# Optimization experiments

Measured on AMD Instinct MI355X. Metric: run time of the kernel, lower is better.

The kernel has to match this reference:

```python
import jax, jax.numpy as jnp
import numpy as np

B, S, D, H, L = 16, 1024, 512, 8, 3
NUM_Q, NUM_C, TOTAL_RES = 10000, 300, 2


def setup_inputs() -> dict:
    k = jax.random.split(jax.random.key(0), 20)
    n = lambda i, s, sc=0.02: jax.random.normal(k[i], s, jnp.float32) * sc
    z = lambda: jnp.zeros((D,), jnp.float32)
    o = lambda: jnp.ones((D,), jnp.float32)
    return {
        'in_ex': jax.random.randint(k[0], (B, S), 0, NUM_Q),
        'in_cat': jax.random.randint(k[1], (B, S), 0, NUM_C),
        'in_res': jax.random.randint(k[2], (B, S), 0, 2),
        'in_pos': n(3, (B, S, D)),
        'en_out': n(4, (B, S, D)),
        'E_res': n(5, (TOTAL_RES + 1, D)),
        'E_ex': n(6, (2 * NUM_Q + 1, D)),
        'E_cat': n(7, (2 * NUM_C + 1, D)),
        'g1': o(), 'be1': z(), 'g2': o(), 'be2': z(), 'g3': o(), 'be3': z(),
        'Wq1': n(8, (D, D)), 'bq1': z(), 'Wk1': n(9, (D, D)), 'bk1': z(),
        'Wv1': n(10, (D, D)), 'bv1': z(), 'Wo1': n(11, (D, D)), 'bo1': z(),
        'Wq2': n(12, (D, D)), 'bq2': z(), 'Wk2': n(13, (D, D)), 'bk2': z(),
        'Wv2': n(14, (D, D)), 'bv2': z(), 'Wo2': n(15, (D, D)), 'bo2': z(),
        'fW1': n(16, (D, D)), 'fb1': z(), 'fW2': n(17, (D, D)), 'fb2': z(),
    }


def layer_norm(x, g, b, eps=1e-5):
    m = x.mean(-1, keepdims=True)
    v = ((x - m) ** 2).mean(-1, keepdims=True)
    return (x - m) / jnp.sqrt(v + eps) * g + b


def pyr_attn(q_in, kv_in, Wq, bq, Wk, bk, Wv, bv, Wo, bo):
    # q_in, kv_in: (S, B, D) as in nn.MultiheadAttention convention
    Sq, Bq, Dm = q_in.shape
    dh = Dm // H
    heads = lambda x: x.reshape(x.shape[0], Bq, H, dh).transpose(1, 2, 0, 3)  # (B,H,S,dh)
    qh = heads(q_in @ Wq + bq)
    kh = heads(kv_in @ Wk + bk)
    vh = heads(kv_in @ Wv + bv)
    Skv = kv_in.shape[0]
    i = jnp.arange(Sq)[:, None]
    Ks, Vs, Ms = [], [], []
    for l in range(L):  # pyramid levels: keys/values avg-pooled by 2**l
        f = 2 ** l
        nb = Skv // f
        Ks.append(kh[:, :, :nb * f].reshape(Bq, H, nb, f, dh).mean(3))
        Vs.append(vh[:, :, :nb * f].reshape(Bq, H, nb, f, dh).mean(3))
        # causal: query i may attend pooled block j only if the block ends at or before i
        Ms.append(i >= (jnp.arange(nb)[None, :] + 1) * f - 1)
    K = jnp.concatenate(Ks, 2)
    V = jnp.concatenate(Vs, 2)
    M = jnp.concatenate(Ms, 1)  # (Sq, K_total) multi-level causal mask
    sc = jnp.einsum('bhqd,bhkd->bhqk', qh, K) / np.sqrt(dh).astype(np.float32)
    sc = jnp.where(M[None, None], sc, -1e9)
    a = jax.nn.softmax(sc, -1)
    out = jnp.einsum('bhqk,bhkd->bhqd', a, V)
    return out.transpose(2, 0, 1, 3).reshape(Sq, Bq, Dm) @ Wo + bo


def reference(in_ex, in_cat, in_res, in_pos, en_out, E_res, E_ex, E_cat,
              g1, be1, g2, be2, g3, be3,
              Wq1, bq1, Wk1, bk1, Wv1, bv1, Wo1, bo1,
              Wq2, bq2, Wk2, bk2, Wv2, bv2, Wo2, bo2,
              fW1, fb1, fW2, fb2):
    # embedding sum (first_block=True)
    out = E_res[in_res] + E_ex[in_ex + NUM_Q * in_res] + E_cat[in_cat + NUM_C * in_res] + in_pos
    out = out.transpose(1, 0, 2)  # (S, B, D)
    out = layer_norm(out, g1, be1)
    out = out + pyr_attn(out, out, Wq1, bq1, Wk1, bk1, Wv1, bv1, Wo1, bo1)
    en = layer_norm(en_out.transpose(1, 0, 2), g2, be2)
    out = out + pyr_attn(out, en, Wq2, bq2, Wk2, bk2, Wv2, bv2, Wo2, bo2)
    out = out.transpose(1, 0, 2)  # (B, S, D)
    out = layer_norm(out, g3, be3)
    out = out + (jax.nn.relu(out @ fW1 + fb1) @ fW2 + fb2)
    return out
```

## Files before the change

### kernel.cpp

```cpp
#include <hip/hip_runtime.h>


#define BB 16
#define SS 1024
#define DD 512
#define HH 8
#define DH 64
#define KTOT 1792
#define NROW (BB*SS)

typedef unsigned short u16;
typedef __attribute__((ext_vector_type(8))) u16 u16x8;
typedef __attribute__((ext_vector_type(4))) u16 u16x4;
typedef __attribute__((ext_vector_type(8))) short s16x8;
typedef __attribute__((ext_vector_type(4))) float f32x4;

__device__ __forceinline__ float b2f(u16 u) {
    return __uint_as_float(((unsigned int)u) << 16);
}
__device__ __forceinline__ u16 f2b(float f) {
    unsigned int u = __float_as_uint(f);
    return (u16)((u + 0x7FFF + ((u >> 16) & 1)) >> 16);
}
__device__ __forceinline__ s16x8 u2s8(u16x8 u) {
    union { u16x8 u; s16x8 s; } x; x.u = u; return x.s;
}
__device__ __forceinline__ f32x4 mfma16(s16x8 a, s16x8 b, f32x4 c) {
    return __builtin_amdgcn_mfma_f32_16x16x32_bf16(a, b, c, 0, 0, 0);
}
__device__ __forceinline__ float wave_sum(float v) {
    #pragma unroll
    for (int m = 1; m < 64; m <<= 1) v += __shfl_xor(v, m, 64);
    return v;
}
__device__ __forceinline__ float exp2a(float x) {
    float r;
    asm("v_exp_f32 %0, %1" : "=v"(r) : "v"(x));
    return r;
}
__device__ __forceinline__ unsigned int cvtpk(float a, float b) {
    unsigned int r;
    asm("v_cvt_pk_bf16_f32 %0, %1, %2" : "=v"(r) : "v"(a), "v"(b));
    return r;
}

__global__ __launch_bounds__(256) void embed_ln_k(
    const int* __restrict__ in_ex, const int* __restrict__ in_cat,
    const int* __restrict__ in_res, const float* __restrict__ in_pos,
    const float* __restrict__ E_res, const float* __restrict__ E_ex,
    const float* __restrict__ E_cat, const float* __restrict__ g,
    const float* __restrict__ be, float* __restrict__ out)
{
    int wave = threadIdx.x >> 6, lane = threadIdx.x & 63;
    int row = blockIdx.x * 4 + wave;
    int res = in_res[row];
    int ex  = in_ex[row] + 10000 * res;
    int cat = in_cat[row] + 300 * res;
    int d0 = lane * 8;
    const float* pr = &E_res[(size_t)res * DD + d0];
    const float* pe = &E_ex[(size_t)ex * DD + d0];
    const float* pc = &E_cat[(size_t)cat * DD + d0];
    const float* pp = &in_pos[(size_t)row * DD + d0];
    float x[8]; float s = 0.f;
    #pragma unroll
    for (int j = 0; j < 8; j++) { x[j] = pr[j] + pe[j] + pc[j] + pp[j]; s += x[j]; }
    s = wave_sum(s);
    float mean = s * (1.0f / DD);
    float vs = 0.f;
    #pragma unroll
    for (int j = 0; j < 8; j++) { float d = x[j] - mean; vs += d * d; }
    vs = wave_sum(vs);
    float rstd = rsqrtf(vs * (1.0f / DD) + 1e-5f);
    #pragma unroll
    for (int j = 0; j < 8; j++)
        out[(size_t)row * DD + d0 + j] = (x[j] - mean) * rstd * g[d0 + j] + be[d0 + j];
}

template<bool OUTB>
__global__ __launch_bounds__(256) void ln_k(
    const float* __restrict__ x, const float* __restrict__ g,
    const float* __restrict__ be, void* __restrict__ outv)
{
    int wave = threadIdx.x >> 6, lane = threadIdx.x & 63;
    int row = blockIdx.x * 4 + wave;
    int d0 = lane * 8;
    const float* px = &x[(size_t)row * DD + d0];
    float xv[8]; float s = 0.f;
    #pragma unroll
    for (int j = 0; j < 8; j++) { xv[j] = px[j]; s += xv[j]; }
    s = wave_sum(s);
    float mean = s * (1.0f / DD);
    float vs = 0.f;
    #pragma unroll
    for (int j = 0; j < 8; j++) { float d = xv[j] - mean; vs += d * d; }
    vs = wave_sum(vs);
    float rstd = rsqrtf(vs * (1.0f / DD) + 1e-5f);
    #pragma unroll
    for (int j = 0; j < 8; j++) {
        float v = (xv[j] - mean) * rstd * g[d0 + j] + be[d0 + j];
        if (OUTB) ((u16*)outv)[(size_t)row * DD + d0 + j] = f2b(v);
        else      ((float*)outv)[(size_t)row * DD + d0 + j] = v;
    }
}

__global__ __launch_bounds__(256) void transpose_k(const float* __restrict__ src, u16* __restrict__ dst)
{
    int idx = blockIdx.x * 256 + threadIdx.x;
    int n = idx & 511, k = idx >> 9;
    dst[n * 512 + k] = f2b(src[k * 512 + n]);
}

__global__ __launch_bounds__(256) void pool_k12_k(u16* __restrict__ KP)
{
    int idx = blockIdx.x * 256 + threadIdx.x;
    int d = idx & 63;
    int t = idx >> 6;
    int k12 = t % 768;
    int bh = t / 768;
    int s0, f;
    if (k12 < 512) { s0 = 2 * k12; f = 2; } else { s0 = 4 * (k12 - 512); f = 4; }
    size_t base = (size_t)bh * KTOT * DH;
    float acc = 0.f;
    for (int i = 0; i < f; i++)
        acc += b2f(KP[base + (size_t)(s0 + i) * DH + d]);
    KP[base + (size_t)(1024 + k12) * DH + d] = f2b(acc * (1.0f / (float)f));
}

__global__ __launch_bounds__(256) void pool_vt_k(const u16* __restrict__ Vp, u16* __restrict__ VPt)
{
    __shared__ __align__(16) u16 T[64 * 72];
    int tid = threadIdx.x;
    int st = blockIdx.x;
    int h  = blockIdx.y;
    int b  = blockIdx.z;
    int s0 = st * 64;
    {
        const u16* src = &Vp[((size_t)(b * SS + s0)) * DD + h * DH];
        #pragma unroll
        for (int it = 0; it < 2; it++) {
            int idx = it * 256 + tid;
            int row = idx >> 3, unit = idx & 7;
            *(u16x8*)&T[row * 72 + unit * 8] =
                *(const u16x8*)&src[(size_t)row * DD + unit * 8];
        }
    }
    __syncthreads();
    int d = tid & 63, g = tid >> 6;
    size_t obase = ((size_t)(b * HH + h) * DH + d) * KTOT;
    #pragma unroll
    for (int gg = 0; gg < 2; gg++) {
        int grp = g * 2 + gg;
        u16x8 v;
        #pragma unroll
        for (int j = 0; j < 8; j++) v[j] = T[(grp * 8 + j) * 72 + d];
        *(u16x8*)&VPt[obase + s0 + grp * 8] = v;
    }
    {
        u16x8 v;
        #pragma unroll
        for (int j = 0; j < 8; j++) {
            int sl = g * 8 + j;
            float a = b2f(T[(2 * sl) * 72 + d]) + b2f(T[(2 * sl + 1) * 72 + d]);
            v[j] = f2b(a * 0.5f);
        }
        *(u16x8*)&VPt[obase + 1024 + st * 32 + g * 8] = v;
    }
    {
        u16x4 v;
        #pragma unroll
        for (int j = 0; j < 4; j++) {
            int s2 = g * 4 + j;
            float a = 0.f;
            #pragma unroll
            for (int i = 0; i < 4; i++) a += b2f(T[(4 * s2 + i) * 72 + d]);
            v[j] = f2b(a * 0.25f);
        }
        *(u16x4*)&VPt[obase + 1536 + st * 16 + g * 4] = v;
    }
}

template<bool AF32, bool RELU, bool RES, bool OUTB, bool KLAY>
__global__ __launch_bounds__(256) void gemm_k(
    const void* __restrict__ Av, const u16* __restrict__ Wt,
    const float* __restrict__ bias, const float* __restrict__ resid,
    void* __restrict__ Cv, int M, int K)
{
    const int N = 512;
    __shared__ __align__(16) u16 As[128 * 40];
    __shared__ __align__(16) u16 Bs[128 * 40];
    int tid = threadIdx.x;
    int wave = tid >> 6, lane = tid & 63;
    int quad = lane >> 4, l16 = lane & 15;
    int m0 = blockIdx.y * 128, n0 = blockIdx.x * 128;
    int wm = (wave >> 1) * 64, wn = (wave & 1) * 64;
    int r = tid >> 1, cg = (tid & 1) * 16;
    f32x4 acc[4][4];
    #pragma unroll
    for (int i = 0; i < 4; i++)
        #pragma unroll
        for (int j = 0; j < 4; j++)
            #pragma unroll
            for (int rr = 0; rr < 4; rr++) acc[i][j][rr] = 0.f;

    for (int k0 = 0; k0 < K; k0 += 32) {
        __syncthreads();
        if (AF32) {
            const float* src = &((const float*)Av)[(size_t)(m0 + r) * K + k0 + cg];
            u16x8 lo, hi;
            #pragma unroll
            for (int j = 0; j < 8; j++) { lo[j] = f2b(src[j]); hi[j] = f2b(src[j + 8]); }
            *(u16x8*)&As[r * 40 + cg] = lo;
            *(u16x8*)&As[r * 40 + cg + 8] = hi;
        } else {
            const u16* src = &((const u16*)Av)[(size_t)(m0 + r) * K + k0 + cg];
            *(u16x8*)&As[r * 40 + cg] = *(const u16x8*)&src[0];
            *(u16x8*)&As[r * 40 + cg + 8] = *(const u16x8*)&src[8];
        }
        {
            const u16* src = &Wt[(size_t)(n0 + r) * K + k0 + cg];
            *(u16x8*)&Bs[r * 40 + cg] = *(const u16x8*)&src[0];
            *(u16x8*)&Bs[r * 40 + cg + 8] = *(const u16x8*)&src[8];
        }
        __syncthreads();
        s16x8 af[4], bfr[4];
        #pragma unroll
        for (int i = 0; i < 4; i++)
            af[i] = u2s8(*(const u16x8*)&As[(wm + i * 16 + l16) * 40 + quad * 8]);
        #pragma unroll
        for (int j = 0; j < 4; j++)
            bfr[j] = u2s8(*(const u16x8*)&Bs[(wn + j * 16 + l16) * 40 + quad * 8]);
        #pragma unroll
        for (int i = 0; i < 4; i++)
            #pragma unroll
            for (int j = 0; j < 4; j++)
                acc[i][j] = mfma16(af[i], bfr[j], acc[i][j]);
    }

    #pragma unroll
    for (int j = 0; j < 4; j++) {
        int col = n0 + wn + j * 16 + l16;
        float bv = bias[col];
        #pragma unroll
        for (int i = 0; i < 4; i++) {
            int rowb = m0 + wm + i * 16 + quad * 4;
            #pragma unroll
            for (int rr = 0; rr < 4; rr++) {
                float v = acc[i][j][rr] + bv;
                if (RELU) v = fmaxf(v, 0.f);
                int row = rowb + rr;
                if (RES) v += resid[(size_t)row * N + col];
                if (KLAY) {
                    int b_ = row >> 10, s_ = row & 1023;
                    size_t dst = (((size_t)(b_ * HH + (col >> 6)) * KTOT) + s_) * DH + (col & 63);
                    ((u16*)Cv)[dst] = f2b(v);
                } else if (OUTB) {
                    ((u16*)Cv)[(size_t)row * N + col] = f2b(v);
                } else {
                    ((float*)Cv)[(size_t)row * N + col] = v;
                }
            }
        }
    }
}

__global__ __launch_bounds__(512) void attn_k(
    const u16* __restrict__ Qp, const u16* __restrict__ KP,
    const u16* __restrict__ VPt, u16* __restrict__ Hout)
{
    __shared__ __align__(16) u16 Ksh[64 * 72];
    __shared__ __align__(16) u16 Vsh[64 * 72];
    int tid = threadIdx.x;
    int wave = tid >> 6, lane = tid & 63;
    int quad = lane >> 4, l16 = lane & 15;
    int id = blockIdx.x;
    int h = id & 7;
    int inner = id >> 3;
    int x = inner & 3, b = inner >> 2;

    int t0 = x + 4 * wave;
    int tiles[2] = { t0, 63 - t0 };

    const u16* Kb = KP  + ((size_t)(b * HH + h)) * KTOT * DH;
    const u16* Vt = VPt + ((size_t)(b * HH + h)) * DH * KTOT;

    s16x8 qa[2][2];
    f32x4 o[2][4];
    float mrun[2] = {-INFINITY, -INFINITY}, lrun[2] = {0.f, 0.f};
    #pragma unroll
    for (int c = 0; c < 2; c++) {
        int q0 = tiles[c] * 16;
        const u16* qrow = Qp + ((size_t)(b * SS + q0 + l16)) * DD + h * DH;
        qa[c][0] = u2s8(*(const u16x8*)&qrow[quad * 8]);
        qa[c][1] = u2s8(*(const u16x8*)&qrow[32 + quad * 8]);
        #pragma unroll
        for (int j = 0; j < 4; j++)
            #pragma unroll
            for (int r = 0; r < 4; r++) o[c][j][r] = 0.f;
    }

    int row0 = 8 * (l16 >> 2) + (l16 & 3);
    const float Cs = 0.18033688f;

    int srow = tid >> 3, sunit = tid & 7;
    u16x8 kreg = *(const u16x8*)&Kb[(size_t)tid * 8];
    u16x8 vreg = *(const u16x8*)&Vt[(size_t)srow * KTOT + sunit * 8];

    for (int ch = 0; ch < 28; ch++) {
        int kbase = ch * 64;
        int lv = (ch < 16) ? 0 : (ch < 24) ? 1 : 2;
        __syncthreads();
        *(u16x8*)&Ksh[srow * 72 + sunit * 8] = kreg;
        *(u16x8*)&Vsh[srow * 72 + sunit * 8] = vreg;
        __syncthreads();
        if (ch + 1 < 28) {
            int nb = (ch + 1) * 64;
            kreg = *(const u16x8*)&Kb[(size_t)nb * DH + tid * 8];
            vreg = *(const u16x8*)&Vt[(size_t)srow * KTOT + nb + sunit * 8];
        }

        #pragma unroll
        for (int c = 0; c < 2; c++) {
            int q0 = tiles[c] * 16;
            int qmax = q0 + 15;
            int efirst = (lv == 0) ? kbase
                       : (lv == 1) ? 2 * (kbase - 1024) + 1
                                   : 4 * (kbase - 1536) + 3;
            if (efirst > qmax) continue;

            int q = q0 + l16;
            int kmax;
            if (lv == 0)      kmax = q - kbase;
            else if (lv == 1) kmax = ((q - 1) >> 1) - (kbase - 1024);
            else              kmax = ((q - 3) >> 2) - (kbase - 1536);
            int thrbase = kmax - 8 * quad;

            float pz[4][4];
            __builtin_amdgcn_s_setprio(1);
            #pragma unroll
            for (int t = 0; t < 4; t++) {
                const int toff = (t & 1) * 4 + (t >> 1) * 32;
                const u16* kr = &Ksh[(row0 + toff) * 72];
                s16x8 kf0 = u2s8(*(const u16x8*)&kr[quad * 8]);
                s16x8 kf1 = u2s8(*(const u16x8*)&kr[32 + quad * 8]);
                f32x4 z;
                #pragma unroll
                for (int r = 0; r < 4; r++) z[r] = 0.f;
                z = mfma16(kf0, qa[c][0], z);
                z = mfma16(kf1, qa[c][1], z);
                int thr = thrbase - toff;
                #pragma unroll
                for (int r = 0; r < 4; r++)
                    pz[t][r] = (r <= thr) ? z[r] : -1e30f;
            }
            __builtin_amdgcn_s_setprio(0);

            float a0 = fmaxf(fmaxf(pz[0][0], pz[0][1]), fmaxf(pz[0][2], pz[0][3]));
            float a1 = fmaxf(fmaxf(pz[1][0], pz[1][1]), fmaxf(pz[1][2], pz[1][3]));
            float a2 = fmaxf(fmaxf(pz[2][0], pz[2][1]), fmaxf(pz[2][2], pz[2][3]));
            float a3 = fmaxf(fmaxf(pz[3][0], pz[3][1]), fmaxf(pz[3][2], pz[3][3]));
            float cmax = fmaxf(fmaxf(a0, a1), fmaxf(a2, a3));
            cmax = fmaxf(cmax, __shfl_xor(cmax, 16, 64));
            cmax = fmaxf(cmax, __shfl_xor(cmax, 32, 64));
            float newm = fmaxf(mrun[c], cmax);
            float nmC = newm * Cs;
            float al = exp2a((mrun[c] - newm) * Cs);
            float p[4][4]; float ps = 0.f;
            #pragma unroll
            for (int t = 0; t < 4; t++)
                #pragma unroll
                for (int r = 0; r < 4; r++) {
                    p[t][r] = exp2a(fmaf(pz[t][r], Cs, -nmC));
                    ps += p[t][r];
                }
            ps += __shfl_xor(ps, 16, 64);
            ps += __shfl_xor(ps, 32, 64);
            lrun[c] = lrun[c] * al + ps;
            mrun[c] = newm;

            float alr[4];
            #pragma unroll
            for (int r = 0; r < 4; r++) alr[r] = __shfl(al, quad * 4 + r, 64);
            #pragma unroll
            for (int j = 0; j < 4; j++)
                #pragma unroll
                for (int r = 0; r < 4; r++) o[c][j][r] *= alr[r];

            union { unsigned int w[4]; u16x8 v; } U0, U1;
            U0.w[0] = cvtpk(p[0][0], p[0][1]); U0.w[1] = cvtpk(p[0][2], p[0][3]);
            U0.w[2] = cvtpk(p[1][0], p[1][1]); U0.w[3] = cvtpk(p[1][2], p[1][3]);
            U1.w[0] = cvtpk(p[2][0], p[2][1]); U1.w[1] = cvtpk(p[2][2], p[2][3]);
            U1.w[2] = cvtpk(p[3][0], p[3][1]); U1.w[3] = cvtpk(p[3][2], p[3][3]);
            s16x8 pf0 = u2s8(U0.v), pf1 = u2s8(U1.v);

            __builtin_amdgcn_s_setprio(1);
            #pragma unroll
            for (int j = 0; j < 4; j++) {
                const u16* vr = &Vsh[(j * 16 + l16) * 72];
                o[c][j] = mfma16(pf0, u2s8(*(const u16x8*)&vr[quad * 8]), o[c][j]);
                o[c][j] = mfma16(pf1, u2s8(*(const u16x8*)&vr[32 + quad * 8]), o[c][j]);
            }
            __builtin_amdgcn_s_setprio(0);
        }
    }

    #pragma unroll
    for (int c = 0; c < 2; c++) {
        int q0 = tiles[c] * 16;
        float il = 1.0f / lrun[c];
        float ilr[4];
        #pragma unroll
        for (int r = 0; r < 4; r++) ilr[r] = __shfl(il, quad * 4 + r, 64);
        #pragma unroll
        for (int r = 0; r < 4; r++) {
            int q = q0 + quad * 4 + r;
            #pragma unroll
            for (int j = 0; j < 4; j++)
                Hout[((size_t)(b * SS + q)) * DD + h * DH + j * 16 + l16] = f2b(o[c][j][r] * ilr[r]);
        }
    }
}

extern "C" void kernel_launch(void* const* d_in, const int* in_sizes, int n_in,
                              void* d_out, int out_size, void* d_ws, size_t ws_size,
                              hipStream_t stream)
{
    (void)in_sizes; (void)n_in; (void)out_size; (void)ws_size;
    const int* in_ex  = (const int*)d_in[0];
    const int* in_cat = (const int*)d_in[1];
    const int* in_res = (const int*)d_in[2];
    const float* in_pos = (const float*)d_in[3];
    const float* en_out = (const float*)d_in[4];
    const float* E_res  = (const float*)d_in[5];
    const float* E_ex   = (const float*)d_in[6];
    const float* E_cat  = (const float*)d_in[7];
    const float* g1 = (const float*)d_in[8],  *be1 = (const float*)d_in[9];
    const float* g2 = (const float*)d_in[10], *be2 = (const float*)d_in[11];
    const float* g3 = (const float*)d_in[12], *be3 = (const float*)d_in[13];
    const float* Wq1 = (const float*)d_in[14], *bq1 = (const float*)d_in[15];
    const float* Wk1 = (const float*)d_in[16], *bk1 = (const float*)d_in[17];
    const float* Wv1 = (const float*)d_in[18], *bv1 = (const float*)d_in[19];
    const float* Wo1 = (const float*)d_in[20], *bo1 = (const float*)d_in[21];
    const float* Wq2 = (const float*)d_in[22], *bq2 = (const float*)d_in[23];
    const float* Wk2 = (const float*)d_in[24], *bk2 = (const float*)d_in[25];
    const float* Wv2 = (const float*)d_in[26], *bv2 = (const float*)d_in[27];
    const float* Wo2 = (const float*)d_in[28], *bo2 = (const float*)d_in[29];
    const float* fW1 = (const float*)d_in[30], *fb1 = (const float*)d_in[31];
    const float* fW2 = (const float*)d_in[32], *fb2 = (const float*)d_in[33];

    char* ws = (char*)d_ws;
    const size_t U = (size_t)NROW * DD * 2;
    float* x1 = (float*)(ws);
    u16* qb   = (u16*)(ws + 2 * U);
    u16* vb   = (u16*)(ws + 3 * U);
    u16* hb   = (u16*)(ws + 4 * U);
    u16* kp   = (u16*)(ws + 5 * U);
    u16* vpt  = (u16*)(ws + 5 * U + 7 * U / 4);
    u16* wt   = (u16*)(ws + 8 * U + U / 2);
    float* x2 = (float*)d_out;
    u16* en = (u16*)(ws);
    float* x3 = x1;
    float* x4 = (float*)(ws + 5 * U);
    u16* ff1 = hb;

    const float* wsrc[10] = {Wq1, Wk1, Wv1, Wo1, Wq2, Wk2, Wv2, Wo2, fW1, fW2};
    for (int i = 0; i < 10; i++)
        transpose_k<<<1024, 256, 0, stream>>>(wsrc[i], wt + (size_t)i * 262144);
    u16* tWq1 = wt,            *tWk1 = wt + 262144,   *tWv1 = wt + 2*262144, *tWo1 = wt + 3*262144;
    u16* tWq2 = wt + 4*262144, *tWk2 = wt + 5*262144, *tWv2 = wt + 6*262144, *tWo2 = wt + 7*262144;
    u16* tF1  = wt + 8*262144, *tF2  = wt + 9*262144;

    dim3 ggrid(4, 128);
    dim3 vtgrid(16, 8, 16);

    embed_ln_k<<<4096, 256, 0, stream>>>(in_ex, in_cat, in_res, in_pos,
                                         E_res, E_ex, E_cat, g1, be1, x1);

    gemm_k<true,false,false,true,false><<<ggrid, 256, 0, stream>>>(x1, tWq1, bq1, nullptr, qb, NROW, 512);
    gemm_k<true,false,false,true,true ><<<ggrid, 256, 0, stream>>>(x1, tWk1, bk1, nullptr, kp, NROW, 512);
    gemm_k<true,false,false,true,false><<<ggrid, 256, 0, stream>>>(x1, tWv1, bv1, nullptr, vb, NROW, 512);
    pool_k12_k<<<24576, 256, 0, stream>>>(kp);
    pool_vt_k<<<vtgrid, 256, 0, stream>>>(vb, vpt);
    attn_k<<<512, 512, 0, stream>>>(qb, kp, vpt, hb);
    gemm_k<false,false,true,false,false><<<ggrid, 256, 0, stream>>>(hb, tWo1, bo1, x1, x2, NROW, 512);

    ln_k<true><<<4096, 256, 0, stream>>>(en_out, g2, be2, en);
    gemm_k<true,false,false,true,false><<<ggrid, 256, 0, stream>>>(x2, tWq2, bq2, nullptr, qb, NROW, 512);
    gemm_k<false,false,false,true,true ><<<ggrid, 256, 0, stream>>>(en, tWk2, bk2, nullptr, kp, NROW, 512);
    gemm_k<false,false,false,true,false><<<ggrid, 256, 0, stream>>>(en, tWv2, bv2, nullptr, vb, NROW, 512);
    pool_k12_k<<<24576, 256, 0, stream>>>(kp);
    pool_vt_k<<<vtgrid, 256, 0, stream>>>(vb, vpt);
    attn_k<<<512, 512, 0, stream>>>(qb, kp, vpt, hb);
    gemm_k<false,false,true,false,false><<<ggrid, 256, 0, stream>>>(hb, tWo2, bo2, x2, x3, NROW, 512);

    ln_k<false><<<4096, 256, 0, stream>>>(x3, g3, be3, x4);
    gemm_k<true,true,false,true,false><<<ggrid, 256, 0, stream>>>(x4, tF1, fb1, nullptr, ff1, NROW, 512);
    gemm_k<false,false,true,false,false><<<ggrid, 256, 0, stream>>>(ff1, tF2, fb2, x4, (float*)d_out, NROW, 512);
}
```

Before: 699.0 us.

## Use direct global-to-LDS loads in GEMM and skip redundant attention masking and rescaling

```diff
diff --git a/kernel.cpp b/kernel.cpp
--- a/kernel.cpp
+++ b/kernel.cpp
@@ -8,6 +8,7 @@
 #define DH 64
 #define KTOT 1792
 #define NROW (BB*SS)
+#define KSW 80
 
 typedef unsigned short u16;
 typedef __attribute__((ext_vector_type(8))) u16 u16x8;
@@ -42,6 +43,12 @@
     unsigned int r;
     asm("v_cvt_pk_bf16_f32 %0, %1, %2" : "=v"(r) : "v"(a), "v"(b));
     return r;
+}
+__device__ __forceinline__ void gl16(const void* g, void* l) {
+    __builtin_amdgcn_global_load_lds(
+        (const __attribute__((address_space(1))) void*)(unsigned long long)g,
+        (__attribute__((address_space(3))) void*)(unsigned int)(unsigned long long)l,
+        16, 0, 0);
 }
 
 __global__ __launch_bounds__(256) void embed_ln_k(
@@ -186,14 +193,17 @@
     void* __restrict__ Cv, int M, int K)
 {
     const int N = 512;
-    __shared__ __align__(16) u16 As[128 * 40];
-    __shared__ __align__(16) u16 Bs[128 * 40];
+    constexpr int ASW = AF32 ? 40 : 32;
+    __shared__ __align__(16) u16 As[128 * ASW];
+    __shared__ __align__(16) u16 Bs[128 * 32];
     int tid = threadIdx.x;
     int wave = tid >> 6, lane = tid & 63;
     int quad = lane >> 4, l16 = lane & 15;
     int m0 = blockIdx.y * 128, n0 = blockIdx.x * 128;
     int wm = (wave >> 1) * 64, wn = (wave & 1) * 64;
     int r = tid >> 1, cg = (tid & 1) * 16;
+    int grow = wave * 16 + (lane >> 2);
+    int gk = (lane & 3) * 8;
     f32x4 acc[4][4];
     #pragma unroll
     for (int i = 0; i < 4; i++)
@@ -206,29 +216,32 @@
         __syncthreads();
         if (AF32) {
             const float* src = &((const float*)Av)[(size_t)(m0 + r) * K + k0 + cg];
-            u16x8 lo, hi;
-            #pragma unroll
-            for (int j = 0; j < 8; j++) { lo[j] = f2b(src[j]); hi[j] = f2b(src[j + 8]); }
-            *(u16x8*)&As[r * 40 + cg] = lo;
-            *(u16x8*)&As[r * 40 + cg + 8] = hi;
+            f32x4 s0 = *(const f32x4*)&src[0];
+            f32x4 s1 = *(const f32x4*)&src[4];
+            f32x4 s2 = *(const f32x4*)&src[8];
+            f32x4 s3 = *(const f32x4*)&src[12];
+            union { unsigned int w[4]; u16x8 v; } L, H;
+            L.w[0] = cvtpk(s0[0], s0[1]); L.w[1] = cvtpk(s0[2], s0[3]);
+            L.w[2] = cvtpk(s1[0], s1[1]); L.w[3] = cvtpk(s1[2], s1[3]);
+            H.w[0] = cvtpk(s2[0], s2[1]); H.w[1] = cvtpk(s2[2], s2[3]);
+            H.w[2] = cvtpk(s3[0], s3[1]); H.w[3] = cvtpk(s3[2], s3[3]);
+            *(u16x8*)&As[r * ASW + cg] = L.v;
+            *(u16x8*)&As[r * ASW + cg + 8] = H.v;
         } else {
-            const u16* src = &((const u16*)Av)[(size_t)(m0 + r) * K + k0 + cg];
-            *(u16x8*)&As[r * 40 + cg] = *(const u16x8*)&src[0];
-            *(u16x8*)&As[r * 40 + cg + 8] = *(const u16x8*)&src[8];
-        }
-        {
-            const u16* src = &Wt[(size_t)(n0 + r) * K + k0 + cg];
-            *(u16x8*)&Bs[r * 40 + cg] = *(const u16x8*)&src[0];
-            *(u16x8*)&Bs[r * 40 + cg + 8] = *(const u16x8*)&src[8];
-        }
+            const u16* Ab = (const u16*)Av;
+            gl16(&Ab[(size_t)(m0 + grow) * K + k0 + gk],      &As[grow * ASW + gk]);
+            gl16(&Ab[(size_t)(m0 + 64 + grow) * K + k0 + gk], &As[(64 + grow) * ASW + gk]);
+        }
+        gl16(&Wt[(size_t)(n0 + grow) * 512 + k0 + gk],      &Bs[grow * 32 + gk]);
+        gl16(&Wt[(size_t)(n0 + 64 + grow) * 512 + k0 + gk], &Bs[(64 + grow) * 32 + gk]);
         __syncthreads();
         s16x8 af[4], bfr[4];
         #pragma unroll
         for (int i = 0; i < 4; i++)
-            af[i] = u2s8(*(const u16x8*)&As[(wm + i * 16 + l16) * 40 + quad * 8]);
+            af[i] = u2s8(*(const u16x8*)&As[(wm + i * 16 + l16) * ASW + quad * 8]);
         #pragma unroll
         for (int j = 0; j < 4; j++)
-            bfr[j] = u2s8(*(const u16x8*)&Bs[(wn + j * 16 + l16) * 40 + quad * 8]);
+            bfr[j] = u2s8(*(const u16x8*)&Bs[(wn + j * 16 + l16) * 32 + quad * 8]);
         #pragma unroll
         for (int i = 0; i < 4; i++)
             #pragma unroll
@@ -267,8 +280,8 @@
     const u16* __restrict__ Qp, const u16* __restrict__ KP,
     const u16* __restrict__ VPt, u16* __restrict__ Hout)
 {
-    __shared__ __align__(16) u16 Ksh[64 * 72];
-    __shared__ __align__(16) u16 Vsh[64 * 72];
+    __shared__ __align__(16) u16 Ksh[64 * KSW];
+    __shared__ __align__(16) u16 Vsh[64 * KSW];
     int tid = threadIdx.x;
     int wave = tid >> 6, lane = tid & 63;
     int quad = lane >> 4, l16 = lane & 15;
@@ -286,6 +299,7 @@
     s16x8 qa[2][2];
     f32x4 o[2][4];
     float mrun[2] = {-INFINITY, -INFINITY}, lrun[2] = {0.f, 0.f};
+    float nmC[2] = {0.f, 0.f};
     #pragma unroll
     for (int c = 0; c < 2; c++) {
         int q0 = tiles[c] * 16;
@@ -309,8 +323,8 @@
         int kbase = ch * 64;
         int lv = (ch < 16) ? 0 : (ch < 24) ? 1 : 2;
         __syncthreads();
-        *(u16x8*)&Ksh[srow * 72 + sunit * 8] = kreg;
-        *(u16x8*)&Vsh[srow * 72 + sunit * 8] = vreg;
+        *(u16x8*)&Ksh[srow * KSW + sunit * 8] = kreg;
+        *(u16x8*)&Vsh[srow * KSW + sunit * 8] = vreg;
         __syncthreads();
         if (ch + 1 < 28) {
             int nb = (ch + 1) * 64;
@@ -327,63 +341,75 @@
                                    : 4 * (kbase - 1536) + 3;
             if (efirst > qmax) continue;
 
-            int q = q0 + l16;
-            int kmax;
-            if (lv == 0)      kmax = q - kbase;
-            else if (lv == 1) kmax = ((q - 1) >> 1) - (kbase - 1024);
-            else              kmax = ((q - 3) >> 2) - (kbase - 1536);
-            int thrbase = kmax - 8 * quad;
-
-            float pz[4][4];
+            int elast = (lv == 0) ? kbase + 63
+                      : (lv == 1) ? 2 * (kbase + 63 - 1024) + 1
+                                  : 4 * (kbase + 63 - 1536) + 3;
+
+            f32x4 zt[4];
             __builtin_amdgcn_s_setprio(1);
             #pragma unroll
             for (int t = 0; t < 4; t++) {
                 const int toff = (t & 1) * 4 + (t >> 1) * 32;
-                const u16* kr = &Ksh[(row0 + toff) * 72];
+                const u16* kr = &Ksh[(row0 + toff) * KSW];
                 s16x8 kf0 = u2s8(*(const u16x8*)&kr[quad * 8]);
                 s16x8 kf1 = u2s8(*(const u16x8*)&kr[32 + quad * 8]);
                 f32x4 z;
                 #pragma unroll
-                for (int r = 0; r < 4; r++) z[r] = 0.f;
+                for (int rr = 0; rr < 4; rr++) z[rr] = 0.f;
                 z = mfma16(kf0, qa[c][0], z);
-                z = mfma16(kf1, qa[c][1], z);
-                int thr = thrbase - toff;
-                #pragma unroll
-                for (int r = 0; r < 4; r++)
-                    pz[t][r] = (r <= thr) ? z[r] : -1e30f;
+                zt[t] = mfma16(kf1, qa[c][1], z);
             }
             __builtin_amdgcn_s_setprio(0);
 
-            float a0 = fmaxf(fmaxf(pz[0][0], pz[0][1]), fmaxf(pz[0][2], pz[0][3]));
-            float a1 = fmaxf(fmaxf(pz[1][0], pz[1][1]), fmaxf(pz[1][2], pz[1][3]));
-            float a2 = fmaxf(fmaxf(pz[2][0], pz[2][1]), fmaxf(pz[2][2], pz[2][3]));
-            float a3 = fmaxf(fmaxf(pz[3][0], pz[3][1]), fmaxf(pz[3][2], pz[3][3]));
+            if (elast > q0) {
+                int q = q0 + l16;
+                int kmaxv = (lv == 0) ? q - kbase
+                          : (lv == 1) ? ((q - 1) >> 1) - (kbase - 1024)
+                                      : ((q - 3) >> 2) - (kbase - 1536);
+                int thrb = kmaxv - 8 * quad;
+                #pragma unroll
+                for (int t = 0; t < 4; t++) {
+                    int thr = thrb - ((t & 1) * 4 + (t >> 1) * 32);
+                    #pragma unroll
+                    for (int rr = 0; rr < 4; rr++)
+                        if (rr > thr) zt[t][rr] = -1e30f;
+                }
+            }
+
+            float a0 = fmaxf(fmaxf(zt[0][0], zt[0][1]), fmaxf(zt[0][2], zt[0][3]));
+            float a1 = fmaxf(fmaxf(zt[1][0], zt[1][1]), fmaxf(zt[1][2], zt[1][3]));
+            float a2 = fmaxf(fmaxf(zt[2][0], zt[2][1]), fmaxf(zt[2][2], zt[2][3]));
+            float a3 = fmaxf(fmaxf(zt[3][0], zt[3][1]), fmaxf(zt[3][2], zt[3][3]));
             float cmax = fmaxf(fmaxf(a0, a1), fmaxf(a2, a3));
             cmax = fmaxf(cmax, __shfl_xor(cmax, 16, 64));
             cmax = fmaxf(cmax, __shfl_xor(cmax, 32, 64));
-            float newm = fmaxf(mrun[c], cmax);
-            float nmC = newm * Cs;
-            float al = exp2a((mrun[c] - newm) * Cs);
+
+            if (__any(cmax > mrun[c])) {
+                float newm = fmaxf(mrun[c], cmax);
+                float al = exp2a((mrun[c] - newm) * Cs);
+                mrun[c] = newm;
+                nmC[c] = newm * Cs;
+                float alr[4];
+                #pragma unroll
+                for (int rr = 0; rr < 4; rr++) alr[rr] = __shfl(al, quad * 4 + rr, 64);
+                #pragma unroll
+                for (int j = 0; j < 4; j++)
+                    #pragma unroll
+                    for (int rr = 0; rr < 4; rr++) o[c][j][rr] *= alr[rr];
+                lrun[c] *= al;
+            }
+
             float p[4][4]; float ps = 0.f;
             #pragma unroll
             for (int t = 0; t < 4; t++)
                 #pragma unroll
-                for (int r = 0; r < 4; r++) {
-                    p[t][r] = exp2a(fmaf(pz[t][r], Cs, -nmC));
-                    ps += p[t][r];
+                for (int rr = 0; rr < 4; rr++) {
+                    p[t][rr] = exp2a(fmaf(zt[t][rr], Cs, -nmC[c]));
+                    ps += p[t][rr];
                 }
             ps += __shfl_xor(ps, 16, 64);
             ps += __shfl_xor(ps, 32, 64);
-            lrun[c] = lrun[c] * al + ps;
-            mrun[c] = newm;
-
-            float alr[4];
-            #pragma unroll
-            for (int r = 0; r < 4; r++) alr[r] = __shfl(al, quad * 4 + r, 64);
-            #pragma unroll
-            for (int j = 0; j < 4; j++)
-                #pragma unroll
-                for (int r = 0; r < 4; r++) o[c][j][r] *= alr[r];
+            lrun[c] += ps;
 
             union { unsigned int w[4]; u16x8 v; } U0, U1;
             U0.w[0] = cvtpk(p[0][0], p[0][1]); U0.w[1] = cvtpk(p[0][2], p[0][3]);
@@ -395,7 +421,7 @@
             __builtin_amdgcn_s_setprio(1);
             #pragma unroll
             for (int j = 0; j < 4; j++) {
-                const u16* vr = &Vsh[(j * 16 + l16) * 72];
+                const u16* vr = &Vsh[(j * 16 + l16) * KSW];
                 o[c][j] = mfma16(pf0, u2s8(*(const u16x8*)&vr[quad * 8]), o[c][j]);
                 o[c][j] = mfma16(pf1, u2s8(*(const u16x8*)&vr[32 + quad * 8]), o[c][j]);
             }
@@ -409,13 +435,13 @@
         float il = 1.0f / lrun[c];
         float ilr[4];
         #pragma unroll
-        for (int r = 0; r < 4; r++) ilr[r] = __shfl(il, quad * 4 + r, 64);
-        #pragma unroll
-        for (int r = 0; r < 4; r++) {
-            int q = q0 + quad * 4 + r;
+        for (int rr = 0; rr < 4; rr++) ilr[rr] = __shfl(il, quad * 4 + rr, 64);
+        #pragma unroll
+        for (int rr = 0; rr < 4; rr++) {
+            int q = q0 + quad * 4 + rr;
             #pragma unroll
             for (int j = 0; j < 4; j++)
-                Hout[((size_t)(b * SS + q)) * DD + h * DH + j * 16 + l16] = f2b(o[c][j][r] * ilr[r]);
+                Hout[((size_t)(b * SS + q)) * DD + h * DH + j * 16 + l16] = f2b(o[c][j][rr] * ilr[rr]);
         }
     }
 }
```

Result: no change. 695.2 us (-0.5%).
